# Kernel tuning notes

Hardware: AMD Instinct MI355X
Metric: run time of the kernel (lower is better)

The kernel has to match this reference:

```python
import jax, jax.numpy as jnp
import numpy as np

NUM_GRAPHS = 1024  # fill_max for batch ids; fixed num_segments for jit


def setup_inputs() -> dict:
    key = jax.random.key(0)
    k1, k2 = jax.random.split(key)
    N, D = 1000000, 256
    x = jax.random.normal(k1, (N, D), dtype=jnp.float32)
    batch = jnp.sort(jax.random.randint(k2, (N,), 0, NUM_GRAPHS, dtype=jnp.int64))
    return {"input": x, "batch": batch}


def reference(input, batch):
    # per-node L2 norm over feature dim: [N]
    all_norms = jnp.sqrt(jnp.sum(input.astype(jnp.float32) ** 2, axis=1))
    seg = batch.astype(jnp.int32)
    # segment-reduce: sum of norms and node counts per graph, [NUM_GRAPHS]
    norm_sum = jax.ops.segment_sum(all_norms, seg, num_segments=NUM_GRAPHS)
    counts = jax.ops.segment_sum(jnp.ones_like(all_norms), seg, num_segments=NUM_GRAPHS)
    per_graph = jnp.where(counts > 0, norm_sum / counts, 0.0)
    # original loops b in range(batch.max()) -> graphs 0..max-1 only
    bmax = batch.max().astype(jnp.float32)
    mask = jnp.arange(NUM_GRAPHS, dtype=jnp.float32) < bmax
    norm_mean = jnp.sum(per_graph * mask) / (bmax + 1.0)
    # module returns input unchanged; norm_mean is the recorded statistic
    return input, norm_mean
```

## Files before the change

### kernel.cpp

```cpp
#include <hip/hip_runtime.h>

#define NUM_GRAPHS 1024
#define D 256

__global__ void activs_init_kernel(float* __restrict__ sums, float* __restrict__ cnts) {
    int i = blockIdx.x * blockDim.x + threadIdx.x;
    if (i < NUM_GRAPHS) {
        sums[i] = 0.0f;
        cnts[i] = 0.0f;
    }
}

__global__ __launch_bounds__(256) void activs_main_kernel(
        const float* __restrict__ x, const int* __restrict__ batch,
        float* __restrict__ out, float* __restrict__ sums,
        float* __restrict__ cnts, int N) {
    const int lane = threadIdx.x & 63;
    const int waveId = (blockIdx.x * blockDim.x + threadIdx.x) >> 6;
    const int totalWaves = (gridDim.x * blockDim.x) >> 6;

    const int rowsPerWave = (N + totalWaves - 1) / totalWaves;
    const int r0 = waveId * rowsPerWave;
    const int r1 = min(r0 + rowsPerWave, N);

    float runSum = 0.0f;
    float runCnt = 0.0f;
    int curSeg = -1;

    for (int r = r0; r < r1; ++r) {
        const size_t base = (size_t)r * D;
        float4 v = ((const float4*)(x + base))[lane];
        ((float4*)(out + base))[lane] = v;

        float s = v.x * v.x + v.y * v.y + v.z * v.z + v.w * v.w;
        #pragma unroll
        for (int m = 32; m; m >>= 1) s += __shfl_xor(s, m, 64);

        if (lane == 0) {
            int seg = batch[r];
            if (seg != curSeg) {
                if (runCnt > 0.0f) {
                    atomicAdd(&sums[curSeg], runSum);
                    atomicAdd(&cnts[curSeg], runCnt);
                }
                curSeg = seg;
                runSum = 0.0f;
                runCnt = 0.0f;
            }
            runSum += sqrtf(s);
            runCnt += 1.0f;
        }
    }
    if (lane == 0 && runCnt > 0.0f) {
        atomicAdd(&sums[curSeg], runSum);
        atomicAdd(&cnts[curSeg], runCnt);
    }
}

__global__ __launch_bounds__(1024) void activs_finalize_kernel(
        const float* __restrict__ sums, const float* __restrict__ cnts,
        const int* __restrict__ batch, int N, float* __restrict__ out_scalar) {
    __shared__ float red[16];
    const int i = threadIdx.x;
    const int lane = i & 63;
    const int w = i >> 6;

    const float bmax = (float)batch[N - 1];

    float c = cnts[i];
    float pg = (c > 0.0f) ? (sums[i] / c) : 0.0f;
    float val = (((float)i) < bmax) ? pg : 0.0f;

    #pragma unroll
    for (int m = 32; m; m >>= 1) val += __shfl_xor(val, m, 64);
    if (lane == 0) red[w] = val;
    __syncthreads();

    if (w == 0) {
        float v = (lane < 16) ? red[lane] : 0.0f;
        #pragma unroll
        for (int m = 8; m; m >>= 1) v += __shfl_xor(v, m, 64);
        if (lane == 0) out_scalar[0] = v / (bmax + 1.0f);
    }
}

extern "C" void kernel_launch(void* const* d_in, const int* in_sizes, int n_in,
                              void* d_out, int out_size, void* d_ws, size_t ws_size,
                              hipStream_t stream) {
    const float* x = (const float*)d_in[0];
    const int* batch = (const int*)d_in[1];
    float* out = (float*)d_out;

    const int N = in_sizes[1];

    float* sums = (float*)d_ws;
    float* cnts = sums + NUM_GRAPHS;

    hipLaunchKernelGGL(activs_init_kernel, dim3(4), dim3(256), 0, stream, sums, cnts);

    hipLaunchKernelGGL(activs_main_kernel, dim3(2048), dim3(256), 0, stream,
                       x, batch, out, sums, cnts, N);

    hipLaunchKernelGGL(activs_finalize_kernel, dim3(1), dim3(1024), 0, stream,
                       sums, cnts, batch, N, out + (size_t)N * D);
}
```

Before: 433.5 us.

## Process eight rows per wave iteration with grid-stride loop and chunked segment atomics

```diff
diff --git a/kernel.cpp b/kernel.cpp
--- a/kernel.cpp
+++ b/kernel.cpp
@@ -11,49 +11,94 @@
     }
 }
 
+__device__ __forceinline__ float sq4(const float4 v) {
+    return v.x * v.x + v.y * v.y + v.z * v.z + v.w * v.w;
+}
+
 __global__ __launch_bounds__(256) void activs_main_kernel(
         const float* __restrict__ x, const int* __restrict__ batch,
         float* __restrict__ out, float* __restrict__ sums,
         float* __restrict__ cnts, int N) {
     const int lane = threadIdx.x & 63;
+    const int q = lane >> 4;
+    const int l = lane & 15;
     const int waveId = (blockIdx.x * blockDim.x + threadIdx.x) >> 6;
     const int totalWaves = (gridDim.x * blockDim.x) >> 6;
 
-    const int rowsPerWave = (N + totalWaves - 1) / totalWaves;
-    const int r0 = waveId * rowsPerWave;
-    const int r1 = min(r0 + rowsPerWave, N);
+    const int Nq = N & ~7;
 
-    float runSum = 0.0f;
-    float runCnt = 0.0f;
-    int curSeg = -1;
+    for (int r0 = waveId * 8; r0 < Nq; r0 += totalWaves * 8) {
+        const float4* srcA = (const float4*)(x + (size_t)(r0 + q) * D);
+        const float4* srcB = (const float4*)(x + (size_t)(r0 + 4 + q) * D);
+        float4* dstA = (float4*)(out + (size_t)(r0 + q) * D);
+        float4* dstB = (float4*)(out + (size_t)(r0 + 4 + q) * D);
 
-    for (int r = r0; r < r1; ++r) {
-        const size_t base = (size_t)r * D;
-        float4 v = ((const float4*)(x + base))[lane];
-        ((float4*)(out + base))[lane] = v;
+        float4 a0 = srcA[l];
+        float4 a1 = srcA[l + 16];
+        float4 a2 = srcA[l + 32];
+        float4 a3 = srcA[l + 48];
+        float4 b0 = srcB[l];
+        float4 b1 = srcB[l + 16];
+        float4 b2 = srcB[l + 32];
+        float4 b3 = srcB[l + 48];
 
-        float s = v.x * v.x + v.y * v.y + v.z * v.z + v.w * v.w;
+        dstA[l]      = a0;
+        dstA[l + 16] = a1;
+        dstA[l + 32] = a2;
+        dstA[l + 48] = a3;
+        dstB[l]      = b0;
+        dstB[l + 16] = b1;
+        dstB[l + 32] = b2;
+        dstB[l + 48] = b3;
+
+        float sA = sq4(a0) + sq4(a1) + sq4(a2) + sq4(a3);
+        float sB = sq4(b0) + sq4(b1) + sq4(b2) + sq4(b3);
         #pragma unroll
-        for (int m = 32; m; m >>= 1) s += __shfl_xor(s, m, 64);
+        for (int m = 1; m <= 8; m <<= 1) {
+            sA += __shfl_xor(sA, m, 64);
+            sB += __shfl_xor(sB, m, 64);
+        }
+        sA = sqrtf(sA);
+        sB = sqrtf(sB);
+
+        float n0 = __shfl(sA, 0, 64), n1 = __shfl(sA, 16, 64);
+        float n2 = __shfl(sA, 32, 64), n3 = __shfl(sA, 48, 64);
+        float n4 = __shfl(sB, 0, 64), n5 = __shfl(sB, 16, 64);
+        float n6 = __shfl(sB, 32, 64), n7 = __shfl(sB, 48, 64);
 
         if (lane == 0) {
-            int seg = batch[r];
-            if (seg != curSeg) {
-                if (runCnt > 0.0f) {
-                    atomicAdd(&sums[curSeg], runSum);
-                    atomicAdd(&cnts[curSeg], runCnt);
+            float n[8] = {n0, n1, n2, n3, n4, n5, n6, n7};
+            const int4 w0 = ((const int4*)(batch + r0))[0];
+            const int4 w1 = ((const int4*)(batch + r0))[1];
+            const int b[8] = {w0.x, w0.y, w0.z, w0.w, w1.x, w1.y, w1.z, w1.w};
+            int seg = b[0];
+            float rs = n[0], rc = 1.0f;
+            #pragma unroll
+            for (int k = 1; k < 8; ++k) {
+                if (b[k] == seg) { rs += n[k]; rc += 1.0f; }
+                else {
+                    atomicAdd(&sums[seg], rs);
+                    atomicAdd(&cnts[seg], rc);
+                    seg = b[k]; rs = n[k]; rc = 1.0f;
                 }
-                curSeg = seg;
-                runSum = 0.0f;
-                runCnt = 0.0f;
             }
-            runSum += sqrtf(s);
-            runCnt += 1.0f;
+            atomicAdd(&sums[seg], rs);
+            atomicAdd(&cnts[seg], rc);
         }
     }
-    if (lane == 0 && runCnt > 0.0f) {
-        atomicAdd(&sums[curSeg], runSum);
-        atomicAdd(&cnts[curSeg], runCnt);
+
+    if (waveId == 0) {
+        for (int r = Nq; r < N; ++r) {
+            const float4 v = ((const float4*)(x + (size_t)r * D))[lane];
+            ((float4*)(out + (size_t)r * D))[lane] = v;
+            float s = sq4(v);
+            #pragma unroll
+            for (int m = 32; m; m >>= 1) s += __shfl_xor(s, m, 64);
+            if (lane == 0) {
+                atomicAdd(&sums[batch[r]], sqrtf(s));
+                atomicAdd(&cnts[batch[r]], 1.0f);
+            }
+        }
     }
 }
 
```

After: 427.3 us. Within noise of the previous version (-1.4%).

## Grid-stride 4-row groups with triple-buffered register prefetch in main kernel

Applied to the files above, without the earlier changes.

```diff
diff --git a/kernel.cpp b/kernel.cpp
--- a/kernel.cpp
+++ b/kernel.cpp
@@ -11,49 +11,115 @@
     }
 }
 
+__device__ __forceinline__ float sq4(const float4 v) {
+    return v.x * v.x + v.y * v.y + v.z * v.z + v.w * v.w;
+}
+
+struct R4 {
+    float4 v0, v1, v2, v3;
+};
+
+__device__ __forceinline__ void load4(R4& R, const float* __restrict__ x,
+                                      int r0, int q, int l) {
+    const float4* src = (const float4*)(x + (size_t)(r0 + q) * D);
+    R.v0 = src[l];
+    R.v1 = src[l + 16];
+    R.v2 = src[l + 32];
+    R.v3 = src[l + 48];
+}
+
+__device__ __forceinline__ void store4(const R4& R, float* __restrict__ out,
+                                       int r0, int q, int l) {
+    float4* dst = (float4*)(out + (size_t)(r0 + q) * D);
+    dst[l]      = R.v0;
+    dst[l + 16] = R.v1;
+    dst[l + 32] = R.v2;
+    dst[l + 48] = R.v3;
+}
+
 __global__ __launch_bounds__(256) void activs_main_kernel(
         const float* __restrict__ x, const int* __restrict__ batch,
         float* __restrict__ out, float* __restrict__ sums,
         float* __restrict__ cnts, int N) {
     const int lane = threadIdx.x & 63;
+    const int q = lane >> 4;
+    const int l = lane & 15;
     const int waveId = (blockIdx.x * blockDim.x + threadIdx.x) >> 6;
     const int totalWaves = (gridDim.x * blockDim.x) >> 6;
+    const int S = totalWaves * 4;
 
-    const int rowsPerWave = (N + totalWaves - 1) / totalWaves;
-    const int r0 = waveId * rowsPerWave;
-    const int r1 = min(r0 + rowsPerWave, N);
+    const int Nq = N & ~3;
+    const int r0 = waveId * 4;
 
-    float runSum = 0.0f;
-    float runCnt = 0.0f;
-    int curSeg = -1;
+    const int k = (r0 < Nq) ? ((Nq - r0 - 4) / S + 1) : 0;
 
-    for (int r = r0; r < r1; ++r) {
-        const size_t base = (size_t)r * D;
-        float4 v = ((const float4*)(x + base))[lane];
-        ((float4*)(out + base))[lane] = v;
+    if (k > 0) {
+        R4 A, B, C;
+        int4 wa, wb, wc;
 
-        float s = v.x * v.x + v.y * v.y + v.z * v.z + v.w * v.w;
-        #pragma unroll
-        for (int m = 32; m; m >>= 1) s += __shfl_xor(s, m, 64);
+        load4(A, x, r0, q, l);
+        wa = *(const int4*)(batch + r0);
+        if (k > 1) {
+            load4(B, x, r0 + S, q, l);
+            wb = *(const int4*)(batch + r0 + S);
+        }
 
-        if (lane == 0) {
-            int seg = batch[r];
-            if (seg != curSeg) {
-                if (runCnt > 0.0f) {
-                    atomicAdd(&sums[curSeg], runSum);
-                    atomicAdd(&cnts[curSeg], runCnt);
+        int r = r0;
+        #pragma unroll 3
+        for (int i = 0; i < k; ++i) {
+            if (i + 2 < k) {
+                load4(C, x, r + 2 * S, q, l);
+                wc = *(const int4*)(batch + r + 2 * S);
+            }
+
+            store4(A, out, r, q, l);
+
+            float s = sq4(A.v0) + sq4(A.v1) + sq4(A.v2) + sq4(A.v3);
+            #pragma unroll
+            for (int m = 1; m <= 8; m <<= 1) s += __shfl_xor(s, m, 64);
+            s = sqrtf(s);
+
+            const float n0 = __shfl(s, 0, 64);
+            const float n1 = __shfl(s, 16, 64);
+            const float n2 = __shfl(s, 32, 64);
+            const float n3 = __shfl(s, 48, 64);
+
+            if (lane == 0) {
+                const float n[4] = {n0, n1, n2, n3};
+                const int b[4] = {wa.x, wa.y, wa.z, wa.w};
+                int seg = b[0];
+                float rs = n[0], rc = 1.0f;
+                #pragma unroll
+                for (int t = 1; t < 4; ++t) {
+                    if (b[t] == seg) { rs += n[t]; rc += 1.0f; }
+                    else {
+                        atomicAdd(&sums[seg], rs);
+                        atomicAdd(&cnts[seg], rc);
+                        seg = b[t]; rs = n[t]; rc = 1.0f;
+                    }
                 }
-                curSeg = seg;
-                runSum = 0.0f;
-                runCnt = 0.0f;
+                atomicAdd(&sums[seg], rs);
+                atomicAdd(&cnts[seg], rc);
             }
-            runSum += sqrtf(s);
-            runCnt += 1.0f;
+
+            A = B; wa = wb;
+            B = C; wb = wc;
+            r += S;
         }
     }
-    if (lane == 0 && runCnt > 0.0f) {
-        atomicAdd(&sums[curSeg], runSum);
-        atomicAdd(&cnts[curSeg], runCnt);
+
+    if (waveId == 0) {
+        for (int t = Nq; t < N; ++t) {
+            const float4 v = ((const float4*)(x + (size_t)t * D))[lane];
+            ((float4*)(out + (size_t)t * D))[lane] = v;
+            float s = sq4(v);
+            #pragma unroll
+            for (int m = 32; m; m >>= 1) s += __shfl_xor(s, m, 64);
+            if (lane == 0) {
+                atomicAdd(&sums[batch[t]], sqrtf(s));
+                atomicAdd(&cnts[batch[t]], 1.0f);
+            }
+        }
     }
 }
 
```

Result: slower. 449.3 us (+3.7%).
